# Optimization experiments

Hardware: AMD Instinct MI355X
Metric: run time of the kernel (lower is better)

The kernel has to match this reference:

```python
import jax, jax.numpy as jnp
import numpy as np

E, F, H = 8, 5632, 2048
T = 8192


def setup_inputs() -> dict:
    key = jax.random.key(0)
    k1, k2, k3, k4 = jax.random.split(key, 4)
    s_w = 1.0 / np.sqrt(H)
    return {
        "expert_idx": 3,
        "hidden_states": jax.random.normal(k1, (T, H), dtype=jnp.float32),
        "fc1_1": jax.random.normal(k2, (E, F, H), dtype=jnp.float32) * s_w,
        "fc1_2": jax.random.normal(k3, (E, F, H), dtype=jnp.float32) * s_w,
        "fc2": jax.random.normal(k4, (E, H, F), dtype=jnp.float32) * (1.0 / np.sqrt(F)),
    }


def reference(expert_idx, hidden_states, fc1_1, fc1_2, fc2):
    # Select this expert's weights: [F,H], [F,H], [H,F]
    w1 = fc1_1[expert_idx]
    w2 = fc1_2[expert_idx]
    w3 = fc2[expert_idx]
    # SwiGLU FFN: silu(x @ w1^T) * (x @ w2^T) @ w3^T
    gate = jnp.einsum("th,fh->tf", hidden_states, w1)
    up = jnp.einsum("th,fh->tf", hidden_states, w2)
    fc1_out = jax.nn.silu(gate) * up  # [T, F]
    out = jnp.einsum("tf,hf->th", fc1_out, w3)  # [T, H]
    return out
```

## Files before the change

kernel.cpp:

```cpp
#include <hip/hip_runtime.h>
#include <hip/hip_bf16.h>

#define T_DIM 8192
#define H_DIM 2048
#define F_DIM 5632

typedef __attribute__((ext_vector_type(4))) float f32x4;
typedef __attribute__((ext_vector_type(8))) short bf16x8;

static __device__ __forceinline__ void gload16(const void* g, void* l) {
    __builtin_amdgcn_global_load_lds(
        (const __attribute__((address_space(1))) void*)g,
        (__attribute__((address_space(3))) void*)l,
        16, 0, 0);
}

static __device__ __forceinline__ unsigned short f2bf(float f) {
    unsigned int u = __float_as_uint(f);
    u += 0x7fffu + ((u >> 16) & 1u);
    return (unsigned short)(u >> 16);
}

__global__ __launch_bounds__(256)
void cvt_x(const float* __restrict__ src, unsigned short* __restrict__ dst, long n)
{
    const long stride = (long)gridDim.x * blockDim.x;
    for (long i = (long)blockIdx.x * blockDim.x + threadIdx.x; i * 4 < n; i += stride) {
        const float4 v = *(const float4*)(src + i * 4);
        ushort4 o;
        o.x = f2bf(v.x); o.y = f2bf(v.y); o.z = f2bf(v.z); o.w = f2bf(v.w);
        *(ushort4*)(dst + i * 4) = o;
    }
}

__global__ __launch_bounds__(256)
void cvt_w(const float* __restrict__ w1, const float* __restrict__ w2,
           const float* __restrict__ w3, const int* __restrict__ eidx,
           unsigned short* __restrict__ W12, unsigned short* __restrict__ W3b)
{
    const long seg = (long)F_DIM * H_DIM;
    const long e   = (long)(*eidx);
    const long nchunks = 3 * seg / 4;
    const long stride = (long)gridDim.x * blockDim.x;
    for (long i = (long)blockIdx.x * blockDim.x + threadIdx.x; i < nchunks; i += stride) {
        const long t = i * 4;
        const int  s = (int)(t / seg);
        const long o = t - (long)s * seg;
        const float4 v = *(const float4*)((s == 0 ? w1 : s == 1 ? w2 : w3) + e * seg + o);
        ushort4 ov;
        ov.x = f2bf(v.x); ov.y = f2bf(v.y); ov.z = f2bf(v.z); ov.w = f2bf(v.w);
        if (s == 2) {
            *(ushort4*)(W3b + o) = ov;
        } else {
            const long r   = o >> 11;
            const long col = o & 2047;
            const int  l7  = (int)(r & 127);
            const long R   = (r >> 7) * 256 + (l7 >> 5) * 64 + (l7 & 31)
                           + (s == 1 ? 32 : 0);
            *(ushort4*)(W12 + R * 2048 + col) = ov;
        }
    }
}

static __device__ __forceinline__ void stage_half(const unsigned short* __restrict__ g,
                                                  long grow0, long ldk, long kb,
                                                  unsigned short* l, int t, int i0)
{
    const int r  = t >> 3;
    const int cc = ((t & 7) ^ (r & 7)) << 3;
    #pragma unroll
    for (int i = i0; i < i0 + 2; ++i)
        gload16(g + (grow0 + i * 64 + r) * ldk + kb + cc,
                l + i * 4096 + t * 8);
}

static __device__ __forceinline__ bf16x8 ldsfrag(const unsigned short* base,
                                                 int row, int kk, int q)
{
    return *(const bf16x8*)(base + row * 64 + (((kk * 4 + q) ^ (row & 7)) << 3));
}

#define PHASE_BODY(p, STAGE_STMT)                                              \
    {                                                                          \
        bf16x8 af[2][2];                                                       \
        _Pragma("unroll")                                                      \
        for (int l_ = 0; l_ < 2; ++l_)                                         \
            _Pragma("unroll")                                                  \
            for (int kk = 0; kk < 2; ++kk)                                     \
                af[l_][kk] = ldsfrag(la, wm * 128 + (p) * 32 + l_ * 16 + lr, kk, q); \
        STAGE_STMT;                                                            \
        __builtin_amdgcn_s_barrier();                                          \
        __builtin_amdgcn_s_setprio(1);                                         \
        _Pragma("unroll")                                                      \
        for (int l_ = 0; l_ < 2; ++l_)                                         \
            _Pragma("unroll")                                                  \
            for (int ni = 0; ni < 4; ++ni)                                     \
                _Pragma("unroll")                                              \
                for (int kk = 0; kk < 2; ++kk)                                 \
                    acc[(p) * 2 + l_][ni] = __builtin_amdgcn_mfma_f32_16x16x32_bf16( \
                        af[l_][kk], bf[ni][kk], acc[(p) * 2 + l_][ni], 0, 0, 0);     \
        __builtin_amdgcn_s_setprio(0);                                         \
        __builtin_amdgcn_s_barrier();                                          \
    }

__global__ __launch_bounds__(512, 2)
void gemm_fc1(const unsigned short* __restrict__ X,
              const unsigned short* __restrict__ W12,
              unsigned short* __restrict__ Hout)
{
    constexpr int NK = H_DIM / 64;

    __shared__ __align__(16) unsigned short sAll[4 * 16384];

    const int tid  = threadIdx.x;
    const int lane = tid & 63;
    const int wid  = tid >> 6;
    const int wm   = wid >> 2;
    const int wn   = wid & 3;
    const int q    = lane >> 4;
    const int lr   = lane & 15;

    const int bid = blockIdx.x;
    const int x   = bid & 7;
    const int i   = bid >> 3;
    const int bn  = i >> 2;
    const int bm  = x * 4 + (i & 3);

    const long arow0 = (long)bm * 256;
    const long brow0 = (long)bn * 256;

    f32x4 acc[8][4] = {};

    stage_half(X,   arow0, H_DIM, 0,  sAll,          tid, 0);
    stage_half(X,   arow0, H_DIM, 0,  sAll,          tid, 2);
    stage_half(W12, brow0, H_DIM, 0,  sAll + 16384,  tid, 0);
    stage_half(W12, brow0, H_DIM, 0,  sAll + 16384,  tid, 2);
    stage_half(W12, brow0, H_DIM, 64, sAll + 49152,  tid, 0);
    stage_half(W12, brow0, H_DIM, 64, sAll + 49152,  tid, 2);

    for (int j = 0; j < NK; ++j) {
        unsigned short* la = sAll + (j & 1) * 32768;
        unsigned short* lb = la + 16384;

        if (j + 1 < NK) {
            unsigned short* na = sAll + ((j + 1) & 1) * 32768;
            stage_half(X, arow0, H_DIM, (long)(j + 1) * 64, na, tid, 0);
            stage_half(X, arow0, H_DIM, (long)(j + 1) * 64, na, tid, 2);
            asm volatile("s_waitcnt vmcnt(8)" ::: "memory");
        } else {
            asm volatile("s_waitcnt vmcnt(0)" ::: "memory");
        }
        __builtin_amdgcn_s_barrier();

        bf16x8 bf[4][2];
        #pragma unroll
        for (int ni = 0; ni < 4; ++ni)
            #pragma unroll
            for (int kk = 0; kk < 2; ++kk)
                bf[ni][kk] = ldsfrag(lb, wn * 64 + ni * 16 + lr, kk, q);

        PHASE_BODY(0, {})
        PHASE_BODY(1, { if (j + 2 < NK) stage_half(W12, brow0, H_DIM, (long)(j + 2) * 64, lb, tid, 0); })
        PHASE_BODY(2, { if (j + 2 < NK) stage_half(W12, brow0, H_DIM, (long)(j + 2) * 64, lb, tid, 2); })
        PHASE_BODY(3, {})
    }

    const long orow = (long)bm * 256 + wm * 128;
    const long ocol = (long)bn * 128 + wn * 32;
    #pragma unroll
    for (int mi = 0; mi < 8; ++mi)
        #pragma unroll
        for (int nj = 0; nj < 2; ++nj)
            #pragma unroll
            for (int r = 0; r < 4; ++r) {
                const float g = acc[mi][nj][r];
                const float u = acc[mi][nj + 2][r];
                const float h = __fdividef(g, 1.0f + __expf(-g)) * u;
                Hout[(orow + mi * 16 + q * 4 + r) * (long)F_DIM +
                     (ocol + nj * 16 + lr)] = f2bf(h);
            }
}

__global__ __launch_bounds__(512, 2)
void gemm_out(const unsigned short* __restrict__ A,
              const unsigned short* __restrict__ B,
              float* __restrict__ Out)
{
    constexpr int NK  = F_DIM / 64;
    constexpr int NBN = H_DIM / 256;

    __shared__ __align__(16) unsigned short sAll[4 * 16384];

    const int tid  = threadIdx.x;
    const int lane = tid & 63;
    const int wid  = tid >> 6;
    const int wm   = wid >> 2;
    const int wn   = wid & 3;
    const int q    = lane >> 4;
    const int lr   = lane & 15;

    const int nwg = gridDim.x;
    const int bid = blockIdx.x;
    const int cpx = nwg >> 3;
    const int swz = (bid & 7) * cpx + (bid >> 3);
    const int bm  = swz / NBN;
    const int bn  = swz % NBN;

    const long arow0 = (long)bm * 256;
    const long brow0 = (long)bn * 256;

    f32x4 acc[8][4] = {};

    stage_half(A, arow0, F_DIM, 0,  sAll,          tid, 0);
    stage_half(A, arow0, F_DIM, 0,  sAll,          tid, 2);
    stage_half(B, brow0, F_DIM, 0,  sAll + 16384,  tid, 0);
    stage_half(B, brow0, F_DIM, 0,  sAll + 16384,  tid, 2);
    stage_half(B, brow0, F_DIM, 64, sAll + 49152,  tid, 0);
    stage_half(B, brow0, F_DIM, 64, sAll + 49152,  tid, 2);

    for (int j = 0; j < NK; ++j) {
        unsigned short* la = sAll + (j & 1) * 32768;
        unsigned short* lb = la + 16384;

        if (j + 1 < NK) {
            unsigned short* na = sAll + ((j + 1) & 1) * 32768;
            stage_half(A, arow0, F_DIM, (long)(j + 1) * 64, na, tid, 0);
            stage_half(A, arow0, F_DIM, (long)(j + 1) * 64, na, tid, 2);
            asm volatile("s_waitcnt vmcnt(8)" ::: "memory");
        } else {
            asm volatile("s_waitcnt vmcnt(0)" ::: "memory");
        }
        __builtin_amdgcn_s_barrier();

        bf16x8 bf[4][2];
        #pragma unroll
        for (int ni = 0; ni < 4; ++ni)
            #pragma unroll
            for (int kk = 0; kk < 2; ++kk)
                bf[ni][kk] = ldsfrag(lb, wn * 64 + ni * 16 + lr, kk, q);

        PHASE_BODY(0, {})
        PHASE_BODY(1, { if (j + 2 < NK) stage_half(B, brow0, F_DIM, (long)(j + 2) * 64, lb, tid, 0); })
        PHASE_BODY(2, { if (j + 2 < NK) stage_half(B, brow0, F_DIM, (long)(j + 2) * 64, lb, tid, 2); })
        PHASE_BODY(3, {})
    }

    const long orow = (long)bm * 256 + wm * 128;
    const long ocol = (long)bn * 256 + wn * 64;
    #pragma unroll
    for (int mi = 0; mi < 8; ++mi)
        #pragma unroll
        for (int ni = 0; ni < 4; ++ni)
            #pragma unroll
            for (int r = 0; r < 4; ++r)
                Out[(orow + mi * 16 + q * 4 + r) * (long)H_DIM + (ocol + ni * 16 + lr)]
                    = acc[mi][ni][r];
}

extern "C" void kernel_launch(void* const* d_in, const int* in_sizes, int n_in,
                              void* d_out, int out_size, void* d_ws, size_t ws_size,
                              hipStream_t stream)
{
    const int*   eidx = (const int*)d_in[0];
    const float* x    = (const float*)d_in[1];
    const float* w1   = (const float*)d_in[2];
    const float* w2   = (const float*)d_in[3];
    const float* w3   = (const float*)d_in[4];
    float* out = (float*)d_out;

    const size_t SZ_X = (size_t)T_DIM * H_DIM;
    const size_t SZ_W = (size_t)F_DIM * H_DIM;

    unsigned short* Xb  = (unsigned short*)d_ws;
    unsigned short* W12 = Xb  + SZ_X;
    unsigned short* W3b = W12 + 2 * SZ_W;
    unsigned short* Hb  = W3b + SZ_W;

    cvt_x<<<2048, 256, 0, stream>>>(x, Xb, (long)SZ_X);
    cvt_w<<<2048, 256, 0, stream>>>(w1, w2, w3, eidx, W12, W3b);

    gemm_fc1<<<(T_DIM / 256) * (F_DIM / 128), 512, 0, stream>>>(Xb, W12, Hb);
    gemm_out<<<(T_DIM / 256) * (H_DIM / 256), 512, 0, stream>>>(Hb, W3b, out);
}
```

Measured before the change: 551.8 us.

## Make fc1 GEMM persistent with one block per CU streaming multiple N tiles

The fc1 GEMM now launches 256 blocks instead of one per output tile. Each block owns one 256-row M tile and walks 5 or 6 consecutive N tiles as a single continuous K loop, so the double-buffered prefetch carries across tile boundaries. The SwiGLU epilogue and accumulator reset run inside the loop at each tile end. This removes the partial last wave and the per-tile pipeline fill and drain. In exchange it halves resident blocks per CU, leaves a 6-versus-5 tile imbalance between blocks, and puts epilogue stores in the path of the MFMA stream.

```diff
diff --git a/kernel.cpp b/kernel.cpp
--- a/kernel.cpp
+++ b/kernel.cpp
@@ -108,8 +108,6 @@
               const unsigned short* __restrict__ W12,
               unsigned short* __restrict__ Hout)
 {
-    constexpr int NK = H_DIM / 64;
-
     __shared__ __align__(16) unsigned short sAll[4 * 16384];
 
     const int tid  = threadIdx.x;
@@ -122,30 +120,33 @@
 
     const int bid = blockIdx.x;
     const int x   = bid & 7;
-    const int i   = bid >> 3;
-    const int bn  = i >> 2;
-    const int bm  = x * 4 + (i & 3);
+    const int c   = bid >> 3;
+    const int bm  = x * 4 + (c & 3);
+    const int g   = c >> 2;
+    const int bn0 = (g < 4) ? 6 * g : 24 + 5 * (g - 4);
+    const int ntt = (g < 4) ? 6 : 5;
+    const int FTOT = ntt * 32;
 
     const long arow0 = (long)bm * 256;
-    const long brow0 = (long)bn * 256;
 
     f32x4 acc[8][4] = {};
 
-    stage_half(X,   arow0, H_DIM, 0,  sAll,          tid, 0);
-    stage_half(X,   arow0, H_DIM, 0,  sAll,          tid, 2);
-    stage_half(W12, brow0, H_DIM, 0,  sAll + 16384,  tid, 0);
-    stage_half(W12, brow0, H_DIM, 0,  sAll + 16384,  tid, 2);
-    stage_half(W12, brow0, H_DIM, 64, sAll + 49152,  tid, 0);
-    stage_half(W12, brow0, H_DIM, 64, sAll + 49152,  tid, 2);
-
-    for (int j = 0; j < NK; ++j) {
-        unsigned short* la = sAll + (j & 1) * 32768;
+    stage_half(X,   arow0,            H_DIM, 0,  sAll,          tid, 0);
+    stage_half(X,   arow0,            H_DIM, 0,  sAll,          tid, 2);
+    stage_half(W12, (long)bn0 * 256,  H_DIM, 0,  sAll + 16384,  tid, 0);
+    stage_half(W12, (long)bn0 * 256,  H_DIM, 0,  sAll + 16384,  tid, 2);
+    stage_half(W12, (long)bn0 * 256,  H_DIM, 64, sAll + 49152,  tid, 0);
+    stage_half(W12, (long)bn0 * 256,  H_DIM, 64, sAll + 49152,  tid, 2);
+
+    for (int f = 0; f < FTOT; ++f) {
+        unsigned short* la = sAll + (f & 1) * 32768;
         unsigned short* lb = la + 16384;
 
-        if (j + 1 < NK) {
-            unsigned short* na = sAll + ((j + 1) & 1) * 32768;
-            stage_half(X, arow0, H_DIM, (long)(j + 1) * 64, na, tid, 0);
-            stage_half(X, arow0, H_DIM, (long)(j + 1) * 64, na, tid, 2);
+        if (f + 1 < FTOT) {
+            unsigned short* na = sAll + ((f + 1) & 1) * 32768;
+            const long kbn = (long)((f + 1) & 31) * 64;
+            stage_half(X, arow0, H_DIM, kbn, na, tid, 0);
+            stage_half(X, arow0, H_DIM, kbn, na, tid, 2);
             asm volatile("s_waitcnt vmcnt(8)" ::: "memory");
         } else {
             asm volatile("s_waitcnt vmcnt(0)" ::: "memory");
@@ -160,25 +161,38 @@
                 bf[ni][kk] = ldsfrag(lb, wn * 64 + ni * 16 + lr, kk, q);
 
         PHASE_BODY(0, {})
-        PHASE_BODY(1, { if (j + 2 < NK) stage_half(W12, brow0, H_DIM, (long)(j + 2) * 64, lb, tid, 0); })
-        PHASE_BODY(2, { if (j + 2 < NK) stage_half(W12, brow0, H_DIM, (long)(j + 2) * 64, lb, tid, 2); })
+        PHASE_BODY(1, { if (f + 2 < FTOT) {
+                            const long br2 = (long)(bn0 + ((f + 2) >> 5)) * 256;
+                            const long kb2 = (long)((f + 2) & 31) * 64;
+                            stage_half(W12, br2, H_DIM, kb2, lb, tid, 0); } })
+        PHASE_BODY(2, { if (f + 2 < FTOT) {
+                            const long br2 = (long)(bn0 + ((f + 2) >> 5)) * 256;
+                            const long kb2 = (long)((f + 2) & 31) * 64;
+                            stage_half(W12, br2, H_DIM, kb2, lb, tid, 2); } })
         PHASE_BODY(3, {})
-    }
-
-    const long orow = (long)bm * 256 + wm * 128;
-    const long ocol = (long)bn * 128 + wn * 32;
-    #pragma unroll
-    for (int mi = 0; mi < 8; ++mi)
-        #pragma unroll
-        for (int nj = 0; nj < 2; ++nj)
-            #pragma unroll
-            for (int r = 0; r < 4; ++r) {
-                const float g = acc[mi][nj][r];
-                const float u = acc[mi][nj + 2][r];
-                const float h = __fdividef(g, 1.0f + __expf(-g)) * u;
-                Hout[(orow + mi * 16 + q * 4 + r) * (long)F_DIM +
-                     (ocol + nj * 16 + lr)] = f2bf(h);
+
+        if ((f & 31) == 31) {
+            const int bn = bn0 + (f >> 5);
+            const long orow = arow0 + wm * 128;
+            const long ocol = (long)bn * 128 + wn * 32;
+            #pragma unroll
+            for (int mi = 0; mi < 8; ++mi) {
+                #pragma unroll
+                for (int nj = 0; nj < 2; ++nj)
+                    #pragma unroll
+                    for (int r = 0; r < 4; ++r) {
+                        const float gv = acc[mi][nj][r];
+                        const float uv = acc[mi][nj + 2][r];
+                        const float h  = __fdividef(gv, 1.0f + __expf(-gv)) * uv;
+                        Hout[(orow + mi * 16 + q * 4 + r) * (long)F_DIM +
+                             (ocol + nj * 16 + lr)] = f2bf(h);
+                    }
+                #pragma unroll
+                for (int ni = 0; ni < 4; ++ni)
+                    acc[mi][ni] = (f32x4){0.f, 0.f, 0.f, 0.f};
             }
+        }
+    }
 }
 
 __global__ __launch_bounds__(512, 2)
@@ -279,6 +293,6 @@
     cvt_x<<<2048, 256, 0, stream>>>(x, Xb, (long)SZ_X);
     cvt_w<<<2048, 256, 0, stream>>>(w1, w2, w3, eidx, W12, W3b);
 
-    gemm_fc1<<<(T_DIM / 256) * (F_DIM / 128), 512, 0, stream>>>(Xb, W12, Hb);
-    gemm_out<<<(T_DIM / 256) * (H_DIM / 256), 512, 0, stream>>>(Hb, W3b, out);
-}
+    gemm_fc1<<<256, 512, 0, stream>>>(Xb, W12, Hb);
+    gemm_out<<<256, 512, 0, stream>>>(Hb, W3b, out);
+}
```

Result: slower. 568.2 us (+3.0%).

## Shrink fc1 GEMM tile to 256x128 with single-buffered weights and higher occupancy

Applied to the files above, without the earlier changes.

Re-interleaves the gate and up weight rows in 16-row groups and rewrites the fc1 GEMM to use a 256x128 tile (64 output F columns) instead of 256x256. The weight tile is single-buffered and the kernel requests 4 blocks per CU via launch bounds, which cuts LDS and accumulator use and doubles the grid size. The aim is more waves in flight to hide latency. The cost is lower arithmetic reuse per block, more global traffic for X, and possible register pressure or spills under the tighter register budget.

```diff
diff --git a/kernel.cpp b/kernel.cpp
--- a/kernel.cpp
+++ b/kernel.cpp
@@ -54,9 +54,7 @@
         } else {
             const long r   = o >> 11;
             const long col = o & 2047;
-            const int  l7  = (int)(r & 127);
-            const long R   = (r >> 7) * 256 + (l7 >> 5) * 64 + (l7 & 31)
-                           + (s == 1 ? 32 : 0);
+            const long R   = (r >> 4) * 32 + (r & 15) + (s == 1 ? 16 : 0);
             *(ushort4*)(W12 + R * 2048 + col) = ov;
         }
     }
@@ -69,15 +67,112 @@
     const int r  = t >> 3;
     const int cc = ((t & 7) ^ (r & 7)) << 3;
     #pragma unroll
-    for (int i = i0; i < i0 + 2; ++i)
-        gload16(g + (grow0 + i * 64 + r) * ldk + kb + cc,
-                l + i * 4096 + t * 8);
+    for (int ii = i0; ii < i0 + 2; ++ii)
+        gload16(g + (grow0 + ii * 64 + r) * ldk + kb + cc,
+                l + ii * 4096 + t * 8);
 }
 
 static __device__ __forceinline__ bf16x8 ldsfrag(const unsigned short* base,
                                                  int row, int kk, int q)
 {
     return *(const bf16x8*)(base + row * 64 + (((kk * 4 + q) ^ (row & 7)) << 3));
+}
+
+#define FC1_PHASE(p, STAGE_STMT)                                               \
+    {                                                                          \
+        bf16x8 af[2][2];                                                       \
+        _Pragma("unroll")                                                      \
+        for (int l_ = 0; l_ < 2; ++l_)                                         \
+            _Pragma("unroll")                                                  \
+            for (int kk = 0; kk < 2; ++kk)                                     \
+                af[l_][kk] = ldsfrag(la, wm * 128 + (p) * 32 + l_ * 16 + lr, kk, q); \
+        STAGE_STMT;                                                            \
+        __builtin_amdgcn_s_barrier();                                          \
+        __builtin_amdgcn_s_setprio(1);                                         \
+        _Pragma("unroll")                                                      \
+        for (int l_ = 0; l_ < 2; ++l_)                                         \
+            _Pragma("unroll")                                                  \
+            for (int nb = 0; nb < 2; ++nb)                                     \
+                _Pragma("unroll")                                              \
+                for (int kk = 0; kk < 2; ++kk)                                 \
+                    acc[(p) * 2 + l_][nb] = __builtin_amdgcn_mfma_f32_16x16x32_bf16( \
+                        af[l_][kk], bf[nb][kk], acc[(p) * 2 + l_][nb], 0, 0, 0);     \
+        __builtin_amdgcn_s_setprio(0);                                         \
+        __builtin_amdgcn_s_barrier();                                          \
+    }
+
+__global__ __launch_bounds__(512, 4)
+void gemm_fc1(const unsigned short* __restrict__ X,
+              const unsigned short* __restrict__ W12,
+              unsigned short* __restrict__ Hout)
+{
+    constexpr int NK = H_DIM / 64;
+
+    __shared__ __align__(16) unsigned short sAll[40960];
+
+    const int tid  = threadIdx.x;
+    const int lane = tid & 63;
+    const int wid  = tid >> 6;
+    const int wm   = wid >> 2;
+    const int wn   = wid & 3;
+    const int q    = lane >> 4;
+    const int lr   = lane & 15;
+
+    const int bid = blockIdx.x;
+    const int x   = bid & 7;
+    const int ii  = bid >> 3;
+    const int bn  = ii >> 2;
+    const int bm  = x * 4 + (ii & 3);
+
+    const long arow0 = (long)bm * 256;
+    const long brow0 = (long)bn * 128;
+
+    unsigned short* sB = sAll + 32768;
+
+    f32x4 acc[8][2] = {};
+
+    stage_half(X,   arow0, H_DIM, 0, sAll, tid, 0);
+    stage_half(X,   arow0, H_DIM, 0, sAll, tid, 2);
+    stage_half(W12, brow0, H_DIM, 0, sB,   tid, 0);
+
+    for (int j = 0; j < NK; ++j) {
+        unsigned short* la = sAll + (j & 1) * 16384;
+
+        if (j + 1 < NK) {
+            unsigned short* na = sAll + ((j + 1) & 1) * 16384;
+            stage_half(X, arow0, H_DIM, (long)(j + 1) * 64, na, tid, 0);
+            stage_half(X, arow0, H_DIM, (long)(j + 1) * 64, na, tid, 2);
+            asm volatile("s_waitcnt vmcnt(4)" ::: "memory");
+        } else {
+            asm volatile("s_waitcnt vmcnt(0)" ::: "memory");
+        }
+        __builtin_amdgcn_s_barrier();
+
+        bf16x8 bf[2][2];
+        #pragma unroll
+        for (int nb = 0; nb < 2; ++nb)
+            #pragma unroll
+            for (int kk = 0; kk < 2; ++kk)
+                bf[nb][kk] = ldsfrag(sB, wn * 32 + nb * 16 + lr, kk, q);
+
+        FC1_PHASE(0, {})
+        FC1_PHASE(1, { if (j + 1 < NK)
+                           stage_half(W12, brow0, H_DIM, (long)(j + 1) * 64, sB, tid, 0); })
+        FC1_PHASE(2, {})
+        FC1_PHASE(3, {})
+    }
+
+    const long orow = (long)bm * 256 + wm * 128;
+    const long ocol = (long)bn * 64 + wn * 16 + lr;
+    #pragma unroll
+    for (int mi = 0; mi < 8; ++mi)
+        #pragma unroll
+        for (int r = 0; r < 4; ++r) {
+            const float g = acc[mi][0][r];
+            const float u = acc[mi][1][r];
+            const float h = __fdividef(g, 1.0f + __expf(-g)) * u;
+            Hout[(orow + mi * 16 + q * 4 + r) * (long)F_DIM + ocol] = f2bf(h);
+        }
 }
 
 #define PHASE_BODY(p, STAGE_STMT)                                              \
@@ -104,84 +199,6 @@
     }
 
 __global__ __launch_bounds__(512, 2)
-void gemm_fc1(const unsigned short* __restrict__ X,
-              const unsigned short* __restrict__ W12,
-              unsigned short* __restrict__ Hout)
-{
-    constexpr int NK = H_DIM / 64;
-
-    __shared__ __align__(16) unsigned short sAll[4 * 16384];
-
-    const int tid  = threadIdx.x;
-    const int lane = tid & 63;
-    const int wid  = tid >> 6;
-    const int wm   = wid >> 2;
-    const int wn   = wid & 3;
-    const int q    = lane >> 4;
-    const int lr   = lane & 15;
-
-    const int bid = blockIdx.x;
-    const int x   = bid & 7;
-    const int i   = bid >> 3;
-    const int bn  = i >> 2;
-    const int bm  = x * 4 + (i & 3);
-
-    const long arow0 = (long)bm * 256;
-    const long brow0 = (long)bn * 256;
-
-    f32x4 acc[8][4] = {};
-
-    stage_half(X,   arow0, H_DIM, 0,  sAll,          tid, 0);
-    stage_half(X,   arow0, H_DIM, 0,  sAll,          tid, 2);
-    stage_half(W12, brow0, H_DIM, 0,  sAll + 16384,  tid, 0);
-    stage_half(W12, brow0, H_DIM, 0,  sAll + 16384,  tid, 2);
-    stage_half(W12, brow0, H_DIM, 64, sAll + 49152,  tid, 0);
-    stage_half(W12, brow0, H_DIM, 64, sAll + 49152,  tid, 2);
-
-    for (int j = 0; j < NK; ++j) {
-        unsigned short* la = sAll + (j & 1) * 32768;
-        unsigned short* lb = la + 16384;
-
-        if (j + 1 < NK) {
-            unsigned short* na = sAll + ((j + 1) & 1) * 32768;
-            stage_half(X, arow0, H_DIM, (long)(j + 1) * 64, na, tid, 0);
-            stage_half(X, arow0, H_DIM, (long)(j + 1) * 64, na, tid, 2);
-            asm volatile("s_waitcnt vmcnt(8)" ::: "memory");
-        } else {
-            asm volatile("s_waitcnt vmcnt(0)" ::: "memory");
-        }
-        __builtin_amdgcn_s_barrier();
-
-        bf16x8 bf[4][2];
-        #pragma unroll
-        for (int ni = 0; ni < 4; ++ni)
-            #pragma unroll
-            for (int kk = 0; kk < 2; ++kk)
-                bf[ni][kk] = ldsfrag(lb, wn * 64 + ni * 16 + lr, kk, q);
-
-        PHASE_BODY(0, {})
-        PHASE_BODY(1, { if (j + 2 < NK) stage_half(W12, brow0, H_DIM, (long)(j + 2) * 64, lb, tid, 0); })
-        PHASE_BODY(2, { if (j + 2 < NK) stage_half(W12, brow0, H_DIM, (long)(j + 2) * 64, lb, tid, 2); })
-        PHASE_BODY(3, {})
-    }
-
-    const long orow = (long)bm * 256 + wm * 128;
-    const long ocol = (long)bn * 128 + wn * 32;
-    #pragma unroll
-    for (int mi = 0; mi < 8; ++mi)
-        #pragma unroll
-        for (int nj = 0; nj < 2; ++nj)
-            #pragma unroll
-            for (int r = 0; r < 4; ++r) {
-                const float g = acc[mi][nj][r];
-                const float u = acc[mi][nj + 2][r];
-                const float h = __fdividef(g, 1.0f + __expf(-g)) * u;
-                Hout[(orow + mi * 16 + q * 4 + r) * (long)F_DIM +
-                     (ocol + nj * 16 + lr)] = f2bf(h);
-            }
-}
-
-__global__ __launch_bounds__(512, 2)
 void gemm_out(const unsigned short* __restrict__ A,
               const unsigned short* __restrict__ B,
               float* __restrict__ Out)
@@ -279,6 +296,6 @@
     cvt_x<<<2048, 256, 0, stream>>>(x, Xb, (long)SZ_X);
     cvt_w<<<2048, 256, 0, stream>>>(w1, w2, w3, eidx, W12, W3b);
 
-    gemm_fc1<<<(T_DIM / 256) * (F_DIM / 128), 512, 0, stream>>>(Xb, W12, Hb);
+    gemm_fc1<<<32 * 88 * 8 / 8 * 8 / 8, 512, 0, stream>>>(Xb, W12, Hb);
     gemm_out<<<(T_DIM / 256) * (H_DIM / 256), 512, 0, stream>>>(Hb, W3b, out);
 }
```

Result: faster. 538.5 us (-2.4%).
